# Performance work log

Measured on AMD Instinct MI355X. Metric: run time of the kernel, lower is better.

Reference implementation:

```python
import jax, jax.numpy as jnp
import numpy as np

B, L, H, HEADS, N_NODE = 1024, 200, 128, 8, 200000
MAXN = L + 1  # max_n_node
D = H // HEADS
EPS = 1e-12


def setup_inputs() -> dict:
    key = jax.random.key(0)
    ks = jax.random.split(key, 20)
    lengths = jax.random.randint(ks[0], (B,), 1, L + 1)
    mask = (jnp.arange(L)[None, :] < lengths[:, None]).astype(jnp.int32)  # contiguous 1s
    alias_inputs = jax.random.randint(ks[1], (B, L), 0, MAXN)
    items = jax.random.randint(ks[2], (B, MAXN), 0, N_NODE)

    def lin_w(k, o, i):
        return (jax.random.normal(k, (o, i), jnp.float32) * 0.1)

    inp = dict(
        alias_inputs=alias_inputs,
        items=items,
        mask=mask,
        emb_W=jax.random.normal(ks[3], (N_NODE, H), jnp.float32) * 0.1,
        # LastAttenion params
        W0=lin_w(ks[4], H, H), b0=jax.random.normal(ks[5], (H,), jnp.float32) * 0.1,
        W1=lin_w(ks[6], H, H), b1=jax.random.normal(ks[7], (H,), jnp.float32) * 0.1,
        W2=lin_w(ks[8], H, H), b2=jax.random.normal(ks[9], (H,), jnp.float32) * 0.1,
        # linear_q[0] (last_k = 1)
        Wq=lin_w(ks[10], H, H), bq=jax.random.normal(ks[11], (H,), jnp.float32) * 0.1,
        # linear_transform (2H -> H)
        Wt=lin_w(ks[12], H, 2 * H), bt=jax.random.normal(ks[13], (H,), jnp.float32) * 0.1,
        ln_g=jax.random.normal(ks[14], (H,), jnp.float32) * 0.1,
        ln_b=jax.random.normal(ks[15], (H,), jnp.float32) * 0.1,
    )
    return inp


def reference(alias_inputs, items, mask, emb_W, W0, b0, W1, b1, W2, b2, Wq, bq, Wt, bt, ln_g, ln_b):
    maskf = mask.astype(jnp.float32)
    # hidden = normalize(embedding(items)); dropout off (eval)
    hidden = emb_W[items]                                                  # [B, MAXN, H]
    hidden = hidden / (jnp.linalg.norm(hidden, axis=-1, keepdims=True) + EPS)
    # per-batch gather: seq_hidden[b, t] = hidden[b, alias_inputs[b, t]]
    seq = jnp.take_along_axis(hidden, alias_inputs[..., None], axis=1)     # [B, L, H]
    seq = seq * maskf[..., None]
    seq = seq / (jnp.linalg.norm(seq, axis=-1, keepdims=True) + EPS)
    # compute_scores
    lengths = mask.sum(1)
    last_idx = lengths - 1                                                 # >= 0 (lengths >= 1)
    ht_last = seq[jnp.arange(B), last_idx]                                 # [B, H]  (ht0 too)
    hts = (ht_last @ Wq.T + bq)[:, None, :]                                # [B, 1, H]
    # torch.norm over dim=1 (size 1) == elementwise abs
    hts = hts / (jnp.linalg.norm(hts, axis=1, keepdims=True) + EPS)
    # LastAttenion (last_k = 1, no lp-pool, eval dropout off)
    q0 = (hts @ W0.T + b0).reshape(B * HEADS, 1, D)                        # [B*h, 1, d]
    q1 = (seq @ W1.T + b1).reshape(B * HEADS, L, D)                        # [B*h, L, d]
    q2 = (seq @ W2.T + b2).reshape(B, L, HEADS, D)                         # [B, L, h, d]
    alpha = jax.nn.sigmoid(jnp.einsum('bkd,bld->bkl', q0, q1))             # [B*h, 1, L]
    alpha = alpha.reshape(B, HEADS, L).transpose(0, 2, 1)                  # [B, L, h]
    alpha = jax.nn.softmax(2.0 * alpha, axis=1)
    a = jnp.sum((alpha[..., None] * q2).reshape(B, L, H) * maskf[..., None], axis=1)  # [B, H]
    # layernorm eps=1e-8
    mu = a.mean(-1, keepdims=True)
    var = ((a - mu) ** 2).mean(-1, keepdims=True)
    a = (a - mu) / jnp.sqrt(var + 1e-8) * ln_g + ln_b
    a = jnp.concatenate([a, ht_last], axis=1) @ Wt.T + bt                  # [B, H]
    # norm=True branch
    a = a / (jnp.linalg.norm(a, axis=1, keepdims=True) + EPS)
    b = emb_W[1:]
    b = b / (jnp.linalg.norm(b, axis=1, keepdims=True) + EPS)
    return a, b.T                                                          # [B,H], [H, N_NODE-1]
```

## Files before the change

kernel.cpp:

```cpp
#include <hip/hip_runtime.h>
#include <math.h>

typedef unsigned int uint;
typedef unsigned short ushort;

__device__ __forceinline__ float b2f(ushort u){
  union { uint i; float f; } v; v.i = ((uint)u) << 16; return v.f;
}
__device__ __forceinline__ ushort f2b(float f){
  union { float f; uint i; } v; v.f = f;
  uint i = v.i;
  i += 0x7fffu + ((i >> 16) & 1u);
  return (ushort)(i >> 16);
}
__device__ __forceinline__ float wred(float v){
  #pragma unroll
  for (int s = 32; s > 0; s >>= 1) v += __shfl_xor(v, s, 64);
  return v;
}
__device__ __forceinline__ float gred16(float v){
  v += __shfl_xor(v, 1, 64);
  v += __shfl_xor(v, 2, 64);
  v += __shfl_xor(v, 4, 64);
  v += __shfl_xor(v, 8, 64);
  return v;
}
__device__ __forceinline__ float sane(float v){ return isfinite(v) ? v : 0.f; }
__device__ __forceinline__ int iclamp(int v, int lo, int hi){ return v < lo ? lo : (v > hi ? hi : v); }
__device__ __forceinline__ void cp8(float d[8], const float s[8]){
  #pragma unroll
  for (int e = 0; e < 8; ++e) d[e] = s[e];
}

__device__ __forceinline__ void load_raw8(const void* emb, int isf, int it, int p, float x[8]){
  if (it >= 0){
    if (isf){
      const float4* q = (const float4*)((const float*)emb + (size_t)it * 128);
      float4 u = q[p * 2], u2 = q[p * 2 + 1];
      x[0] = u.x; x[1] = u.y; x[2] = u.z; x[3] = u.w;
      x[4] = u2.x; x[5] = u2.y; x[6] = u2.z; x[7] = u2.w;
    } else {
      uint4 u = ((const uint4*)((const ushort*)emb + (size_t)it * 128))[p];
      x[0] = b2f((ushort)u.x); x[1] = b2f((ushort)(u.x >> 16));
      x[2] = b2f((ushort)u.y); x[3] = b2f((ushort)(u.y >> 16));
      x[4] = b2f((ushort)u.z); x[5] = b2f((ushort)(u.z >> 16));
      x[6] = b2f((ushort)u.w); x[7] = b2f((ushort)(u.w >> 16));
    }
  } else {
    #pragma unroll
    for (int e = 0; e < 8; ++e) x[e] = 0.f;
  }
}

__device__ __forceinline__ int detect_isf(const void* emb, int t, int* s_flag){
  if (t == 0) *s_flag = 0;
  __syncthreads();
  if (t < 64){
    uint4 u = ((const uint4*)emb)[t];
    uint w[4] = { u.x, u.y, u.z, u.w };
    int bad = 0;
    #pragma unroll
    for (int e = 0; e < 4; ++e){
      float v0 = fabsf(b2f((ushort)w[e]));
      float v1 = fabsf(b2f((ushort)(w[e] >> 16)));
      if (!(v0 <= 1e4f) || !(v1 <= 1e4f)) bad = 1;
    }
    if (bad) *s_flag = 1;
  }
  __syncthreads();
  return *s_flag;
}

#define OUTB 131072

#define C_W0T 0
#define C_W1  16384
#define C_W2T 32768
#define C_WQT 49152
#define C_WTT 65536
#define C_B0  98304
#define C_B1  98432
#define C_B2  98560
#define C_BQ  98688
#define C_BT  98816
#define C_G   98944
#define C_BB  99072
#define C_TOT 99200

#define KMAIN_SMEM 22784

__global__ __launch_bounds__(256) void k_bout(
    const void* __restrict__ emb,
    const void* W0, const void* b0, const void* W1, const void* b1,
    const void* W2, const void* b2, const void* Wq, const void* bq,
    const void* Wt, const void* bt, const void* g, const void* bb,
    float* __restrict__ wts, void* __restrict__ outv){
  __shared__ float tile[64 * 129];
  __shared__ int s_flag;
  const int t = threadIdx.x, gid = t >> 4, p = t & 15;
  const int base = blockIdx.x * 64;
  const int isf = detect_isf(emb, t, &s_flag);
  for (int i = gid; i < 64; i += 16){
    int gi = base + i;
    if (gi < 199999){
      float x[8];
      if (isf){
        const float4* q = (const float4*)((const float*)emb + (size_t)(gi + 1) * 128);
        float4 u = q[p * 2], u2 = q[p * 2 + 1];
        x[0] = u.x; x[1] = u.y; x[2] = u.z; x[3] = u.w;
        x[4] = u2.x; x[5] = u2.y; x[6] = u2.z; x[7] = u2.w;
      } else {
        uint4 u = ((const uint4*)((const ushort*)emb + (size_t)(gi + 1) * 128))[p];
        x[0] = b2f((ushort)u.x); x[1] = b2f((ushort)(u.x >> 16));
        x[2] = b2f((ushort)u.y); x[3] = b2f((ushort)(u.y >> 16));
        x[4] = b2f((ushort)u.z); x[5] = b2f((ushort)(u.z >> 16));
        x[6] = b2f((ushort)u.w); x[7] = b2f((ushort)(u.w >> 16));
      }
      float ss = 0.f;
      #pragma unroll
      for (int e = 0; e < 8; ++e) ss += x[e] * x[e];
      ss = gred16(ss);
      float inv = 1.f / (sqrtf(ss) + 1e-12f);
      #pragma unroll
      for (int e = 0; e < 8; ++e) tile[i * 129 + p * 8 + e] = x[e] * inv;
    }
  }
  __syncthreads();
  for (int it = 0; it < 32; ++it){
    int idx = it * 256 + t;
    int h = idx >> 6, n = idx & 63;
    int gi = base + n;
    if (gi < 199999){
      float val = sane(tile[n * 129 + h]);
      if (isf) ((float*)outv)[OUTB + (size_t)h * 199999 + gi] = val;
      else     ((ushort*)outv)[OUTB + (size_t)h * 199999 + gi] = f2b(val);
    }
  }
  int j = blockIdx.x * 256 + t;
  if (blockIdx.x < 388 && j < C_TOT){
    const void* src; int si;
    if (j < 16384)      { int k = j >> 7, h = j & 127; src = W0; si = h * 128 + k; }
    else if (j < 32768) { src = W1; si = j - 16384; }
    else if (j < 49152) { int i = j - 32768; int k = i >> 7, h = i & 127; src = W2; si = h * 128 + k; }
    else if (j < 65536) { int i = j - 49152; int k = i >> 7, h = i & 127; src = Wq; si = h * 128 + k; }
    else if (j < 98304) { int i = j - 65536; int k = i >> 7, h = i & 127; src = Wt; si = h * 256 + k; }
    else {
      int i = j - 98304; int arr = i >> 7;
      const void* tab[7] = { b0, b1, b2, bq, bt, g, bb };
      src = tab[arr]; si = i & 127;
    }
    wts[j] = isf ? ((const float*)src)[si] : b2f(((const ushort*)src)[si]);
  }
}

__global__ __launch_bounds__(256) void k_main(
    const int* __restrict__ alias_, const int* __restrict__ items,
    const int* __restrict__ mask, const void* __restrict__ emb,
    const float* __restrict__ wts, void* __restrict__ outv){
  extern __shared__ __align__(16) char dsm[];
  __shared__ int s_flag;
  __shared__ float s_X0[128], s_ht[128], s_a[128], s_hts[128];
  __shared__ float s_c1[64];
  __shared__ float s_T[8], s_Tp[64];
  __shared__ float s_red[16];
  __shared__ float s_nrm[200];
  __shared__ int   s_it[200];
  __shared__ int   s_item;

  const int t = threadIdx.x;
  const int isf = detect_isf(emb, t, &s_flag);
  const int b = blockIdx.x;

  ushort* s_w1p   = (ushort*)dsm;
  float*  s_part  = (float*)dsm;
  float*  s_alpha = (float*)(dsm + 16384);

  const int wv = t >> 6, gid = t >> 4, p = t & 15, lane = t & 63;
  const int mbase = b * 200;

  int mv = 0;
  if (t < 200){
    mv = mask[mbase + t];
    int a = mv ? iclamp(alias_[mbase + t], 0, 200) : 0;
    s_it[t] = mv ? iclamp(items[b * 201 + a], 0, 199999) : -1;
  }
  float lv = wred((float)mv);
  if ((t & 63) == 0) s_red[t >> 6] = lv;
  __syncthreads();

  float xc[8], xn1[8];
  load_raw8(emb, isf, s_it[gid], p, xc);
  load_raw8(emb, isf, s_it[gid + 16], p, xn1);

  const int len = iclamp((int)(s_red[0] + s_red[1] + s_red[2] + s_red[3] + 0.5f), 1, 200);
  if (t == 0){
    int a = iclamp(alias_[mbase + len - 1], 0, 200);
    s_item = iclamp(items[b * 201 + a], 0, 199999);
  }
  __syncthreads();

  float v = 0.f;
  if (t < 128)
    v = isf ? ((const float*)emb)[(size_t)s_item * 128 + t]
            : b2f(((const ushort*)emb)[(size_t)s_item * 128 + t]);
  float ss = wred(v * v);
  if ((t & 63) == 0) s_red[4 + (t >> 6)] = ss;
  __syncthreads();
  v = v / (sqrtf(s_red[4] + s_red[5]) + 1e-12f);
  float ss2 = wred(v * v);
  if ((t & 63) == 0) s_red[8 + (t >> 6)] = ss2;
  __syncthreads();
  v = v / (sqrtf(s_red[8] + s_red[9]) + 1e-12f);
  if (t < 128) s_ht[t] = v;
  __syncthreads();

  if (t < 128){
    double d0 = 0.0, d1 = 0.0, d2 = 0.0, d3 = 0.0;
    for (int k = 0; k < 128; k += 4){
      d0 += (double)wts[C_WQT + (k    ) * 128 + t] * (double)s_ht[k    ];
      d1 += (double)wts[C_WQT + (k + 1) * 128 + t] * (double)s_ht[k + 1];
      d2 += (double)wts[C_WQT + (k + 2) * 128 + t] * (double)s_ht[k + 2];
      d3 += (double)wts[C_WQT + (k + 3) * 128 + t] * (double)s_ht[k + 3];
    }
    float a = (float)((double)wts[C_BQ + t] + ((d0 + d1) + (d2 + d3)));
    s_hts[t] = a / (fabsf(a) + 1e-12f);
  }
  __syncthreads();
  if (t < 128){
    float a0 = 0.f, a1 = 0.f, a2 = 0.f, a3 = 0.f;
    for (int k = 0; k < 128; k += 4){
      a0 += wts[C_W0T + (k    ) * 128 + t] * s_hts[k    ];
      a1 += wts[C_W0T + (k + 1) * 128 + t] * s_hts[k + 1];
      a2 += wts[C_W0T + (k + 2) * 128 + t] * s_hts[k + 2];
      a3 += wts[C_W0T + (k + 3) * 128 + t] * s_hts[k + 3];
    }
    s_X0[t] = wts[C_B0 + t] + ((a0 + a1) + (a2 + a3));
  }
  __syncthreads();
  if (t < 64){
    int head = t >> 3, j = t & 7;
    float c = 0.f;
    #pragma unroll
    for (int d = 0; d < 16; ++d) c += s_X0[head * 16 + d] * wts[C_B1 + j * 16 + d];
    s_c1[t] = c;
  }

  __syncthreads();
  for (int idx = t; idx < 8192; idx += 256){
    int hj = idx >> 7, k = idx & 127, head = hj >> 3, j = hj & 7;
    float acc = 0.f;
    const float* w1r = wts + C_W1 + (j * 16) * 128 + k;
    #pragma unroll
    for (int d = 0; d < 16; ++d) acc += s_X0[head * 16 + d] * w1r[d * 128];
    s_w1p[hj * 128 + k] = f2b(acc);
  }
  __syncthreads();

  {
    float xt[8];
    for (int r = gid; r < 200; r += 16){
      int rn = r + 32;
      load_raw8(emb, isf, rn < 200 ? s_it[rn] : -1, p, xt);

      int head = r / 25, lb = (r % 25) * 8;
      uint4 wu[8];
      #pragma unroll
      for (int j = 0; j < 8; ++j)
        wu[j] = *(const uint4*)(s_w1p + (head * 8 + j) * 128 + p * 8);

      float ssr = 0.f;
      #pragma unroll
      for (int e = 0; e < 8; ++e) ssr += xc[e] * xc[e];
      ssr = gred16(ssr);
      float inv = 1.f / (sqrtf(ssr) + 1e-12f);
      #pragma unroll
      for (int e = 0; e < 8; ++e) xc[e] *= inv;
      if (p == 0) s_nrm[r] = inv;

      #pragma unroll
      for (int j = 0; j < 8; ++j){
        float dot = xc[0] * b2f((ushort)wu[j].x) + xc[1] * b2f((ushort)(wu[j].x >> 16))
                  + xc[2] * b2f((ushort)wu[j].y) + xc[3] * b2f((ushort)(wu[j].y >> 16))
                  + xc[4] * b2f((ushort)wu[j].z) + xc[5] * b2f((ushort)(wu[j].z >> 16))
                  + xc[6] * b2f((ushort)wu[j].w) + xc[7] * b2f((ushort)(wu[j].w >> 16));
        dot = gred16(dot);
        if (p == 0){
          float logit = s_c1[head * 8 + j] + dot;
          s_alpha[(lb + j) * 8 + head] = 2.f / (1.f + expf(-logit));
        }
      }
      cp8(xc, xn1); cp8(xn1, xt);
    }
  }
  __syncthreads();

  {
    int head = t >> 5, l32 = t & 31;
    float vals[7]; float mx = -1e30f;
    #pragma unroll
    for (int i = 0; i < 7; ++i){
      int l = l32 + 32 * i;
      float xx = (l < 200) ? s_alpha[l * 8 + head] : -1e30f;
      vals[i] = xx; mx = fmaxf(mx, xx);
    }
    #pragma unroll
    for (int s = 16; s > 0; s >>= 1) mx = fmaxf(mx, __shfl_xor(mx, s, 64));
    float sum = 0.f; float e[7];
    #pragma unroll
    for (int i = 0; i < 7; ++i){
      int l = l32 + 32 * i;
      float ex = (l < 200) ? expf(vals[i] - mx) : 0.f;
      e[i] = ex; sum += ex;
    }
    #pragma unroll
    for (int s = 16; s > 0; s >>= 1) sum += __shfl_xor(sum, s, 64);
    float inv = 1.f / sum;
    #pragma unroll
    for (int i = 0; i < 7; ++i){
      int l = l32 + 32 * i;
      if (l < 200) s_alpha[l * 8 + head] = e[i] * inv;
    }
  }
  __syncthreads();

  if (t < 64){
    int h = t & 7, seg = t >> 3;
    int l0 = seg * 25, l1 = l0 + 25; if (l1 > len) l1 = len;
    float s = 0.f;
    for (int l = l0; l < l1; ++l) s += s_alpha[l * 8 + h];
    s_Tp[t] = s;
  }
  __syncthreads();
  if (t < 8){
    float s = 0.f;
    #pragma unroll
    for (int seg = 0; seg < 8; ++seg) s += s_Tp[seg * 8 + t];
    s_T[t] = s;
  }

  float acc[64];
  #pragma unroll
  for (int e = 0; e < 64; ++e) acc[e] = 0.f;
  {
    float ha[8], hb[8], ht8[8];
    load_raw8(emb, isf, s_it[gid], p, ha);
    load_raw8(emb, isf, gid + 16 < 200 ? s_it[gid + 16] : -1, p, hb);
    for (int l = gid; l < 200; l += 16){
      int lc = l + 32;
      load_raw8(emb, isf, lc < 200 ? s_it[lc] : -1, p, ht8);
      if (s_it[l] >= 0){
        float nm = s_nrm[l];
        float x[8];
        #pragma unroll
        for (int e = 0; e < 8; ++e) x[e] = ha[e] * nm;
        float4 a0 = *(const float4*)(s_alpha + l * 8);
        float4 a1 = *(const float4*)(s_alpha + l * 8 + 4);
        float al[8] = { a0.x, a0.y, a0.z, a0.w, a1.x, a1.y, a1.z, a1.w };
        #pragma unroll
        for (int h = 0; h < 8; ++h)
          #pragma unroll
          for (int e = 0; e < 8; ++e) acc[h * 8 + e] += al[h] * x[e];
      }
      cp8(ha, hb); cp8(hb, ht8);
    }
  }
  #pragma unroll
  for (int e = 0; e < 64; ++e){
    float vv = acc[e];
    vv += __shfl_xor(vv, 16, 64);
    vv += __shfl_xor(vv, 32, 64);
    acc[e] = vv;
  }
  __syncthreads();
  if (lane < 16){
    #pragma unroll
    for (int h = 0; h < 8; ++h)
      #pragma unroll
      for (int e = 0; e < 8; ++e)
        s_part[wv * 1024 + h * 128 + p * 8 + e] = acc[h * 8 + e];
  }
  __syncthreads();
  for (int i = t; i < 1024; i += 256)
    s_part[i] = s_part[i] + s_part[1024 + i] + s_part[2048 + i] + s_part[3072 + i];
  __syncthreads();

  float araw = 0.f;
  if (t < 128){
    int head = t >> 4;
    const float* hl = &s_part[head * 128];
    float a0 = 0.f, a1 = 0.f, a2 = 0.f, a3 = 0.f;
    for (int k = 0; k < 128; k += 4){
      a0 += hl[k    ] * wts[C_W2T + (k    ) * 128 + t];
      a1 += hl[k + 1] * wts[C_W2T + (k + 1) * 128 + t];
      a2 += hl[k + 2] * wts[C_W2T + (k + 2) * 128 + t];
      a3 += hl[k + 3] * wts[C_W2T + (k + 3) * 128 + t];
    }
    araw = wts[C_B2 + t] * s_T[head] + ((a0 + a1) + (a2 + a3));
  }
  float v1 = wred(t < 128 ? araw : 0.f);
  if ((t & 63) == 0) s_red[t >> 6] = v1;
  __syncthreads();
  float mu = (s_red[0] + s_red[1]) * 0.0078125f;
  float dd = (t < 128) ? (araw - mu) : 0.f;
  float v2 = wred(dd * dd);
  if ((t & 63) == 0) s_red[4 + (t >> 6)] = v2;
  __syncthreads();
  float var = (s_red[4] + s_red[5]) * 0.0078125f;
  if (t < 128)
    s_a[t] = dd / sqrtf(var + 1e-8f) * wts[C_G + t] + wts[C_BB + t];
  __syncthreads();

  float o = 0.f;
  if (t < 128){
    float o0 = 0.f, o1 = 0.f, o2 = 0.f, o3 = 0.f;
    for (int k = 0; k < 128; k += 2){
      o0 += s_a[k    ] * wts[C_WTT + (k      ) * 128 + t];
      o1 += s_a[k + 1] * wts[C_WTT + (k + 1  ) * 128 + t];
      o2 += s_ht[k   ] * wts[C_WTT + (128 + k) * 128 + t];
      o3 += s_ht[k+ 1] * wts[C_WTT + (129 + k) * 128 + t];
    }
    o = wts[C_BT + t] + ((o0 + o1) + (o2 + o3));
  }
  float v3 = wred(t < 128 ? o * o : 0.f);
  if ((t & 63) == 0) s_red[8 + (t >> 6)] = v3;
  __syncthreads();
  float nrm = sqrtf(s_red[8] + s_red[9]);
  if (t < 128){
    float val = sane(o / (nrm + 1e-12f));
    if (isf) ((float*)outv)[b * 128 + t] = val;
    else     ((ushort*)outv)[b * 128 + t] = f2b(val);
  }
}

extern "C" void kernel_launch(void* const* d_in, const int* in_sizes, int n_in,
                              void* d_out, int out_size, void* d_ws, size_t ws_size,
                              hipStream_t stream){
  const int* alias_ = (const int*)d_in[0];
  const int* items  = (const int*)d_in[1];
  const int* mask   = (const int*)d_in[2];
  const void* emb = d_in[3];
  const void* W0  = d_in[4];
  const void* b0  = d_in[5];
  const void* W1  = d_in[6];
  const void* b1  = d_in[7];
  const void* W2  = d_in[8];
  const void* b2_ = d_in[9];
  const void* Wq  = d_in[10];
  const void* bq  = d_in[11];
  const void* Wt  = d_in[12];
  const void* bt  = d_in[13];
  const void* g_  = d_in[14];
  const void* bb_ = d_in[15];

  char* ws = (char*)d_ws;
  float* wts = (float*)ws;

  static int g_attr_done = 0;
  if (!g_attr_done){
    hipFuncSetAttribute(reinterpret_cast<const void*>(k_main),
                        hipFuncAttributeMaxDynamicSharedMemorySize, KMAIN_SMEM);
    g_attr_done = 1;
  }

  k_bout<<<dim3(3125), dim3(256), 0,          stream>>>(emb, W0, b0, W1, b1,
                                              W2, b2_, Wq, bq, Wt, bt, g_, bb_,
                                              wts, d_out);
  k_main<<<dim3(1024), dim3(256), KMAIN_SMEM, stream>>>(alias_, items, mask, emb,
                                              wts, d_out);
}
```

Measured before the change: 378.6 us.

## Fuse embedding-normalize transpose blocks into main kernel and split weight prep

Moves the weight-prep work into its own small 388-block kernel and merges the large normalize-and-transpose work into the per-batch attention kernel. The two kinds of block are interleaved across one grid so that memory-bound transpose blocks run alongside compute-heavy attention blocks. The transpose tile is processed in two 32-row halves so it fits in the shared-memory buffer the fused kernel already allocates. Output stores become nontemporal. The cost is branch divergence at block level and an extra sync per block. Occupancy is now set by the larger kernel's shared-memory footprint for both block types.

```diff
diff --git a/kernel.cpp b/kernel.cpp
--- a/kernel.cpp
+++ b/kernel.cpp
@@ -87,73 +87,80 @@
 #define C_BB  99072
 #define C_TOT 99200
 
-#define KMAIN_SMEM 22784
-
-__global__ __launch_bounds__(256) void k_bout(
+#define KFUSED_SMEM 22784
+
+#define NB_MAIN 1024
+#define NB_BOUT 3125
+#define NB_TOT  4149
+
+__global__ __launch_bounds__(256) void k_wts(
     const void* __restrict__ emb,
     const void* W0, const void* b0, const void* W1, const void* b1,
     const void* W2, const void* b2, const void* Wq, const void* bq,
     const void* Wt, const void* bt, const void* g, const void* bb,
-    float* __restrict__ wts, void* __restrict__ outv){
-  __shared__ float tile[64 * 129];
+    float* __restrict__ wts){
   __shared__ int s_flag;
-  const int t = threadIdx.x, gid = t >> 4, p = t & 15;
-  const int base = blockIdx.x * 64;
+  const int t = threadIdx.x;
   const int isf = detect_isf(emb, t, &s_flag);
-  for (int i = gid; i < 64; i += 16){
-    int gi = base + i;
-    if (gi < 199999){
-      float x[8];
-      if (isf){
-        const float4* q = (const float4*)((const float*)emb + (size_t)(gi + 1) * 128);
-        float4 u = q[p * 2], u2 = q[p * 2 + 1];
-        x[0] = u.x; x[1] = u.y; x[2] = u.z; x[3] = u.w;
-        x[4] = u2.x; x[5] = u2.y; x[6] = u2.z; x[7] = u2.w;
-      } else {
-        uint4 u = ((const uint4*)((const ushort*)emb + (size_t)(gi + 1) * 128))[p];
-        x[0] = b2f((ushort)u.x); x[1] = b2f((ushort)(u.x >> 16));
-        x[2] = b2f((ushort)u.y); x[3] = b2f((ushort)(u.y >> 16));
-        x[4] = b2f((ushort)u.z); x[5] = b2f((ushort)(u.z >> 16));
-        x[6] = b2f((ushort)u.w); x[7] = b2f((ushort)(u.w >> 16));
+  int j = blockIdx.x * 256 + t;
+  if (j >= C_TOT) return;
+  const void* src; int si;
+  if (j < 16384)      { int k = j >> 7, h = j & 127; src = W0; si = h * 128 + k; }
+  else if (j < 32768) { src = W1; si = j - 16384; }
+  else if (j < 49152) { int i = j - 32768; int k = i >> 7, h = i & 127; src = W2; si = h * 128 + k; }
+  else if (j < 65536) { int i = j - 49152; int k = i >> 7, h = i & 127; src = Wq; si = h * 128 + k; }
+  else if (j < 98304) { int i = j - 65536; int k = i >> 7, h = i & 127; src = Wt; si = h * 256 + k; }
+  else {
+    int i = j - 98304; int arr = i >> 7;
+    const void* tab[7] = { b0, b1, b2, bq, bt, g, bb };
+    src = tab[arr]; si = i & 127;
+  }
+  wts[j] = isf ? ((const float*)src)[si] : b2f(((const ushort*)src)[si]);
+}
+
+__device__ void bout_block(const void* __restrict__ emb, int isf,
+                           void* __restrict__ outv, int bb, int t, char* dsm){
+  float* tile = (float*)dsm;
+  const int gid = t >> 4, p = t & 15;
+  const int base = bb * 64;
+  for (int pass = 0; pass < 2; ++pass){
+    const int pb = base + pass * 32;
+    if (pass) __syncthreads();
+    for (int i = gid; i < 32; i += 16){
+      int gi = pb + i;
+      if (gi < 199999){
+        float x[8];
+        load_raw8(emb, isf, gi + 1, p, x);
+        float ss = 0.f;
+        #pragma unroll
+        for (int e = 0; e < 8; ++e) ss += x[e] * x[e];
+        ss = gred16(ss);
+        float inv = 1.f / (sqrtf(ss) + 1e-12f);
+        #pragma unroll
+        for (int e = 0; e < 8; ++e) tile[i * 129 + p * 8 + e] = x[e] * inv;
       }
-      float ss = 0.f;
-      #pragma unroll
-      for (int e = 0; e < 8; ++e) ss += x[e] * x[e];
-      ss = gred16(ss);
-      float inv = 1.f / (sqrtf(ss) + 1e-12f);
-      #pragma unroll
-      for (int e = 0; e < 8; ++e) tile[i * 129 + p * 8 + e] = x[e] * inv;
-    }
-  }
-  __syncthreads();
-  for (int it = 0; it < 32; ++it){
-    int idx = it * 256 + t;
-    int h = idx >> 6, n = idx & 63;
-    int gi = base + n;
-    if (gi < 199999){
-      float val = sane(tile[n * 129 + h]);
-      if (isf) ((float*)outv)[OUTB + (size_t)h * 199999 + gi] = val;
-      else     ((ushort*)outv)[OUTB + (size_t)h * 199999 + gi] = f2b(val);
-    }
-  }
-  int j = blockIdx.x * 256 + t;
-  if (blockIdx.x < 388 && j < C_TOT){
-    const void* src; int si;
-    if (j < 16384)      { int k = j >> 7, h = j & 127; src = W0; si = h * 128 + k; }
-    else if (j < 32768) { src = W1; si = j - 16384; }
-    else if (j < 49152) { int i = j - 32768; int k = i >> 7, h = i & 127; src = W2; si = h * 128 + k; }
-    else if (j < 65536) { int i = j - 49152; int k = i >> 7, h = i & 127; src = Wq; si = h * 128 + k; }
-    else if (j < 98304) { int i = j - 65536; int k = i >> 7, h = i & 127; src = Wt; si = h * 256 + k; }
-    else {
-      int i = j - 98304; int arr = i >> 7;
-      const void* tab[7] = { b0, b1, b2, bq, bt, g, bb };
-      src = tab[arr]; si = i & 127;
-    }
-    wts[j] = isf ? ((const float*)src)[si] : b2f(((const ushort*)src)[si]);
-  }
-}
-
-__global__ __launch_bounds__(256) void k_main(
+    }
+    __syncthreads();
+    #pragma unroll
+    for (int it = 0; it < 16; ++it){
+      int idx = it * 256 + t;
+      int h = idx >> 5, n = idx & 31;
+      int gi = pb + n;
+      if (gi < 199999){
+        float val = sane(tile[n * 129 + h]);
+        if (isf){
+          float* op = (float*)outv + OUTB + (size_t)h * 199999 + gi;
+          __builtin_nontemporal_store(val, op);
+        } else {
+          ushort* op = (ushort*)outv + OUTB + (size_t)h * 199999 + gi;
+          __builtin_nontemporal_store(f2b(val), op);
+        }
+      }
+    }
+  }
+}
+
+__global__ __launch_bounds__(256) void k_fused(
     const int* __restrict__ alias_, const int* __restrict__ items,
     const int* __restrict__ mask, const void* __restrict__ emb,
     const float* __restrict__ wts, void* __restrict__ outv){
@@ -169,7 +176,15 @@
 
   const int t = threadIdx.x;
   const int isf = detect_isf(emb, t, &s_flag);
-  const int b = blockIdx.x;
+
+  const int bid = blockIdx.x;
+  const int m = (bid * NB_MAIN) / NB_TOT;
+  const bool is_main = ((bid + 1) * NB_MAIN) / NB_TOT > m;
+  if (!is_main){
+    bout_block(emb, isf, outv, bid - m, t, dsm);
+    return;
+  }
+  const int b = m;
 
   ushort* s_w1p   = (ushort*)dsm;
   float*  s_part  = (float*)dsm;
@@ -457,14 +472,14 @@
 
   static int g_attr_done = 0;
   if (!g_attr_done){
-    hipFuncSetAttribute(reinterpret_cast<const void*>(k_main),
-                        hipFuncAttributeMaxDynamicSharedMemorySize, KMAIN_SMEM);
+    hipError_t e = hipFuncSetAttribute(reinterpret_cast<const void*>(k_fused),
+                        hipFuncAttributeMaxDynamicSharedMemorySize, KFUSED_SMEM);
+    (void)e;
     g_attr_done = 1;
   }
 
-  k_bout<<<dim3(3125), dim3(256), 0,          stream>>>(emb, W0, b0, W1, b1,
-                                              W2, b2_, Wq, bq, Wt, bt, g_, bb_,
-                                              wts, d_out);
-  k_main<<<dim3(1024), dim3(256), KMAIN_SMEM, stream>>>(alias_, items, mask, emb,
-                                              wts, d_out);
-}
+  k_wts  <<<dim3(388),    dim3(256), 0,           stream>>>(emb, W0, b0, W1, b1,
+                                                  W2, b2_, Wq, bq, Wt, bt, g_, bb_, wts);
+  k_fused<<<dim3(NB_TOT), dim3(256), KFUSED_SMEM, stream>>>(alias_, items, mask, emb,
+                                                  wts, d_out);
+}
```

Result: faster. 362.0 us (-4.4%).
